# Kernel optimization log

Hardware: AMD Instinct MI355X
Metric: run time of the kernel (lower is better)

The kernel has to match this reference:

```python
import jax, jax.numpy as jnp
import numpy as np

B, N, DIM, H = 4, 2048, 1024, 8
HD = DIM // H
SCALE = HD ** -0.5


def setup_inputs() -> dict:
    key = jax.random.key(0)
    ks = jax.random.split(key, 9)
    inp = {
        "q": jax.random.normal(ks[0], (B, N, DIM), dtype=jnp.float32),
        "k": jax.random.normal(ks[1], (B, N, DIM), dtype=jnp.float32),
        "v": jax.random.normal(ks[2], (B, N, DIM), dtype=jnp.float32),
        "trans_mat": jax.random.normal(ks[3], (B, N, N), dtype=jnp.float32),
        # torch Linear weights: [out_features, in_features]; qkv_bias=False
        "Wq": jax.random.normal(ks[4], (DIM, DIM), dtype=jnp.float32) * (DIM ** -0.5),
        "Wk": jax.random.normal(ks[5], (DIM, DIM), dtype=jnp.float32) * (DIM ** -0.5),
        "Wv": jax.random.normal(ks[6], (DIM, DIM), dtype=jnp.float32) * (DIM ** -0.5),
        "Wp": jax.random.normal(ks[7], (DIM, DIM), dtype=jnp.float32) * (DIM ** -0.5),
        "bp": jax.random.normal(ks[8], (DIM,), dtype=jnp.float32) * 0.01,
    }
    return inp


def reference(q, k, v, trans_mat, Wq, Wk, Wv, Wp, bp):
    Bq, Nq, C = q.shape
    # project and split heads: [B, H, N, HD]
    qh = (q @ Wq.T).reshape(Bq, Nq, H, HD).transpose(0, 2, 1, 3)
    kh = (k @ Wk.T).reshape(Bq, -1, H, HD).transpose(0, 2, 1, 3)
    vh = (v @ Wv.T).reshape(Bq, -1, H, HD).transpose(0, 2, 1, 3)
    # scaled scores gated elementwise by trans_mat (broadcast over heads)
    scores = jnp.einsum("bhqd,bhkd->bhqk", qh, kh) * SCALE
    gated = scores * trans_mat[:, None, :, :]
    # softmax over full row, then zero out positions where gated == 0
    sm = jax.nn.softmax(gated, axis=-1)
    attn = jnp.where(gated != 0, sm, jnp.zeros((), dtype=sm.dtype))
    x = jnp.einsum("bhqk,bhkd->bhqd", attn, vh)
    x = x.transpose(0, 2, 1, 3).reshape(Bq, Nq, C)
    return x @ Wp.T + bp
```

## Files before the change

kernel.cpp:

```cpp
#include <hip/hip_runtime.h>
#include <hip/hip_bf16.h>
#include <stdint.h>

#define B_    4
#define N_    2048
#define DIM_  1024
#define H_    8
#define HD_   128
#define MTOK  (B_ * N_)
#define SCALE_  0.08838834764831845f
#define LOG2E_  1.4426950408889634f
#define QSCALE_ (SCALE_ * LOG2E_)

typedef unsigned short u16;
typedef __attribute__((ext_vector_type(4)))  float f32x4;
typedef __attribute__((ext_vector_type(16))) float f32x16;
typedef __attribute__((ext_vector_type(8)))  short s16x8;
typedef __attribute__((ext_vector_type(8)))  u16  u16x8;
typedef __attribute__((ext_vector_type(4)))  u16  u16x4;
typedef __attribute__((ext_vector_type(4)))  unsigned u32x4;

__device__ __forceinline__ u16 f2bf(float f) {
    uint32_t i = __builtin_bit_cast(uint32_t, f);
    return (u16)((i + 0x7FFFu + ((i >> 16) & 1u)) >> 16);
}
__device__ __forceinline__ unsigned pk_bf16(float a, float b) {
    unsigned r;
    asm("v_cvt_pk_bf16_f32 %0, %1, %2" : "=v"(r) : "v"(a), "v"(b));
    return r;
}
__device__ __forceinline__ void pl32_swap(unsigned &a, unsigned &b) {
    asm volatile("v_permlane32_swap_b32 %0, %1" : "+v"(a), "+v"(b));
}
__device__ __forceinline__ void gl_lds16(const u16* g, u16* l) {
    __builtin_amdgcn_global_load_lds((const __attribute__((address_space(1))) void*)g,
                                     (__attribute__((address_space(3))) void*)l,
                                     16, 0, 0);
}

__global__ __launch_bounds__(256) void cvt_f32_bf16(const float* __restrict__ src,
                                                    u16* __restrict__ dst, int n) {
    int i = (blockIdx.x * 256 + threadIdx.x) * 4;
    int stride = gridDim.x * 256 * 4;
    for (; i < n; i += stride) {
        float4 v = *(const float4*)(src + i);
        u16x4 o;
        o.x = f2bf(v.x); o.y = f2bf(v.y); o.z = f2bf(v.z); o.w = f2bf(v.w);
        *(u16x4*)(dst + i) = o;
    }
}

__global__ __launch_bounds__(256) void cvt3(const float* __restrict__ q,
                                            const float* __restrict__ k,
                                            const float* __restrict__ v,
                                            u16* __restrict__ qb,
                                            u16* __restrict__ kb,
                                            u16* __restrict__ vb) {
    const float* s = blockIdx.y == 0 ? q : blockIdx.y == 1 ? k : v;
    u16* d = blockIdx.y == 0 ? qb : blockIdx.y == 1 ? kb : vb;
    int i = (blockIdx.x * 256 + threadIdx.x) * 8;
    float4 a = *(const float4*)(s + i);
    float4 b = *(const float4*)(s + i + 4);
    u32x4 w = {pk_bf16(a.x, a.y), pk_bf16(a.z, a.w), pk_bf16(b.x, b.y), pk_bf16(b.z, b.w)};
    *(u16x8*)(d + i) = __builtin_bit_cast(u16x8, w);
}

__global__ __launch_bounds__(256) void cvt_w4(const float* __restrict__ s0,
                                              const float* __restrict__ s1,
                                              const float* __restrict__ s2,
                                              const float* __restrict__ s3,
                                              u16* __restrict__ dst) {
    const float* s = blockIdx.y == 0 ? s0 : blockIdx.y == 1 ? s1 : blockIdx.y == 2 ? s2 : s3;
    u16* d = dst + (size_t)blockIdx.y * (DIM_ * DIM_);
    int i = (blockIdx.x * 256 + threadIdx.x) * 8;
    float4 a = *(const float4*)(s + i);
    float4 b = *(const float4*)(s + i + 4);
    u32x4 w = {pk_bf16(a.x, a.y), pk_bf16(a.z, a.w), pk_bf16(b.x, b.y), pk_bf16(b.z, b.w)};
    *(u16x8*)(d + i) = __builtin_bit_cast(u16x8, w);
}

__global__ __launch_bounds__(256) void transpose_f32(const float* __restrict__ in,
                                                     float* __restrict__ out) {
    __shared__ float t[64][65];
    const int r0 = blockIdx.y * 64, c0 = blockIdx.x * 64;
    const float* ib = in + (size_t)blockIdx.z * N_ * N_;
    float* ob = out + (size_t)blockIdx.z * N_ * N_;
    const int lr = threadIdx.x >> 4;
    const int lc = threadIdx.x & 15;
    #pragma unroll
    for (int i = 0; i < 4; i++) {
        int row = i * 16 + lr;
        float4 v = *(const float4*)(ib + (size_t)(r0 + row) * N_ + c0 + lc * 4);
        t[row][lc * 4 + 0] = v.x; t[row][lc * 4 + 1] = v.y;
        t[row][lc * 4 + 2] = v.z; t[row][lc * 4 + 3] = v.w;
    }
    __syncthreads();
    #pragma unroll
    for (int i = 0; i < 4; i++) {
        int row = i * 16 + lr;
        float4 w;
        w.x = t[lc * 4 + 0][row]; w.y = t[lc * 4 + 1][row];
        w.z = t[lc * 4 + 2][row]; w.w = t[lc * 4 + 3][row];
        *(float4*)(ob + (size_t)(c0 + row) * N_ + r0 + lc * 4) = w;
    }
}

template <int MODE>
__global__ __launch_bounds__(256) void gemm_bt(const u16* __restrict__ A,
                                               const u16* __restrict__ Bt,
                                               void* __restrict__ Cout,
                                               const float* __restrict__ bias,
                                               float scale, int M, int NN, int K) {
    __shared__ __align__(16) u16 lga[128 * 64];
    __shared__ __align__(16) u16 lgb[128 * 64];
    const int tid  = threadIdx.x;
    const int lane = tid & 63, wave = tid >> 6;
    const int wm = wave >> 1, wn = wave & 1;
    int lin = blockIdx.x + gridDim.x * blockIdx.y;
    int w   = (lin & 7) * 64 + (lin >> 3);
    const int row0 = (w >> 3) * 128, col0 = (w & 7) * 128;

    f32x4 acc[4][4] = {};

    auto stageLds = [&](const u16* G, u16* L, int rowbase, int k0) {
        #pragma unroll
        for (int i = 0; i < 4; i++) {
            int rb = wave * 32 + i * 8;
            int r  = rb + (lane >> 3);
            int cc = (lane & 7) ^ (lane >> 3);
            gl_lds16(G + (size_t)(rowbase + r) * K + k0 + cc * 8, L + rb * 64);
        }
    };

    for (int k0 = 0; k0 < K; k0 += 64) {
        stageLds(A,  lga, row0, k0);
        stageLds(Bt, lgb, col0, k0);
        __syncthreads();
        #pragma unroll
        for (int kk = 0; kk < 2; kk++) {
            s16x8 af[4], bfr[4];
            #pragma unroll
            for (int mi = 0; mi < 4; mi++) {
                int r = wm * 64 + mi * 16 + (lane & 15);
                int sc = (kk * 4 + (lane >> 4)) ^ (lane & 7);
                af[mi] = *(const s16x8*)(&lga[r * 64 + sc * 8]);
            }
            #pragma unroll
            for (int ni = 0; ni < 4; ni++) {
                int r = wn * 64 + ni * 16 + (lane & 15);
                int sc = (kk * 4 + (lane >> 4)) ^ (lane & 7);
                bfr[ni] = *(const s16x8*)(&lgb[r * 64 + sc * 8]);
            }
            #pragma unroll
            for (int mi = 0; mi < 4; mi++)
                #pragma unroll
                for (int ni = 0; ni < 4; ni++)
                    acc[mi][ni] = __builtin_amdgcn_mfma_f32_16x16x32_bf16(
                        af[mi], bfr[ni], acc[mi][ni], 0, 0, 0);
        }
        __syncthreads();
    }

    #pragma unroll
    for (int mi = 0; mi < 4; mi++) {
        #pragma unroll
        for (int ni = 0; ni < 4; ni++) {
            #pragma unroll
            for (int r = 0; r < 4; r++) {
                int grow = row0 + wm * 64 + mi * 16 + ((lane >> 4) << 2) + r;
                int gcol = col0 + wn * 64 + ni * 16 + (lane & 15);
                float vv = acc[mi][ni][r];
                if (MODE == 2) {
                    ((float*)Cout)[(size_t)grow * NN + gcol] = vv + bias[gcol];
                } else {
                    vv *= scale;
                    int bb = grow >> 11, n = grow & (N_ - 1);
                    int hh = gcol >> 7,  d = gcol & (HD_ - 1);
                    size_t idx = (MODE == 0)
                        ? ((size_t)(bb * H_ + hh) * N_ + n) * HD_ + d
                        : ((size_t)(bb * H_ + hh) * HD_ + d) * N_ + n;
                    ((u16*)Cout)[idx] = f2bf(vv);
                }
            }
        }
    }
}

__global__ __launch_bounds__(256, 2) void attn_swapped(const u16* __restrict__ Qh,
                                                       const u16* __restrict__ Kh,
                                                       const u16* __restrict__ Vt,
                                                       const float* __restrict__ transT,
                                                       u16* __restrict__ xout) {
    __shared__ __align__(16) u16 kt[2][64 * 128];
    __shared__ __align__(16) u16 vt[2][128 * 64];

    const int tid = threadIdx.x, lane = tid & 63, wave = tid >> 6;
    const int lq = lane & 31, hl = lane >> 5;

    int lin = blockIdx.x + 16 * (blockIdx.y + 8 * blockIdx.z);
    int nl  = (lin & 7) * 64 + (lin >> 3);
    const int qt = nl & 15, hh = (nl >> 4) & 7, b = nl >> 7;
    const int q0 = qt * 128 + wave * 32;
    const int q  = q0 + lq;

    const u16* Qbh = Qh + (size_t)(b * H_ + hh) * N_ * HD_;
    const u16* Kbh = Kh + (size_t)(b * H_ + hh) * N_ * HD_;
    const u16* Vbh = Vt + (size_t)(b * H_ + hh) * HD_ * N_;
    const float* tTq = transT + (size_t)b * N_ * N_ + q;

    s16x8 qf[8];
    #pragma unroll
    for (int s = 0; s < 8; s++)
        qf[s] = *(const s16x8*)(Qbh + (size_t)q * HD_ + s * 16 + hl * 8);

    auto stageKV = [&](int kv0, int bi) {
        #pragma unroll
        for (int i = 0; i < 4; i++) {
            int rk = wave * 16 + i * 4 + (lane >> 4);
            int ck = (lane & 15) ^ (rk & 15) ^ ((rk & 16) >> 2);
            gl_lds16(Kbh + (size_t)(kv0 + rk) * HD_ + ck * 8,
                     &kt[bi][(wave * 16 + i * 4) * 128]);
            int rv = wave * 32 + i * 8 + (lane >> 3);
            int cv = (lane & 7) ^ (rv & 7) ^ ((rv >> 3) & 3);
            gl_lds16(Vbh + (size_t)rv * N_ + kv0 + cv * 8,
                     &vt[bi][(wave * 32 + i * 8) * 64]);
        }
    };

    const int mKl = (lq & 15) ^ ((lq & 16) >> 2);
    const int mVl = (lq & 7) ^ ((lq >> 3) & 3);

    float m = -3.0e38f, l = 0.f;
    f32x16 aoT[4] = {};

    stageKV(0, 0);
    __syncthreads();

    for (int it = 0; it < N_ / 64; it++) {
        const int kv0 = it * 64, cur = it & 1;
        if (it + 1 < N_ / 64) stageKV(kv0 + 64, cur ^ 1);

        float tt[2][16];
        #pragma unroll
        for (int ni = 0; ni < 2; ni++)
            #pragma unroll
            for (int idx = 0; idx < 16; idx++) {
                int kv = (idx & 3) + 8 * (idx >> 2) + 4 * hl + 32 * ni;
                tt[ni][idx] = tTq[(size_t)(kv0 + kv) * N_];
            }

        f32x16 sT[2] = {};
        __builtin_amdgcn_s_setprio(1);
        #pragma unroll
        for (int s = 0; s < 8; s++)
            #pragma unroll
            for (int ni = 0; ni < 2; ni++) {
                int r = ni * 32 + lq;
                int slot = (2 * s + hl) ^ mKl;
                s16x8 kf = *(const s16x8*)(&kt[cur][r * 128 + slot * 8]);
                sT[ni] = __builtin_amdgcn_mfma_f32_32x32x16_bf16(kf, qf[s], sT[ni], 0, 0, 0);
            }
        __builtin_amdgcn_s_setprio(0);

        float mx = -3.0e38f;
        #pragma unroll
        for (int ni = 0; ni < 2; ni++)
            #pragma unroll
            for (int idx = 0; idx < 16; idx++) {
                float g = sT[ni][idx] * tt[ni][idx];
                sT[ni][idx] = g;
                mx = fmaxf(mx, g);
            }
        mx = fmaxf(mx, __shfl_xor(mx, 32));

        if (__any(mx > m + 8.0f)) {
            float mn = fmaxf(m, mx);
            float sfv = __builtin_amdgcn_exp2f(m - mn);
            m = mn;
            l *= sfv;
            #pragma unroll
            for (int dt = 0; dt < 4; dt++)
                #pragma unroll
                for (int e = 0; e < 16; e++) aoT[dt][e] *= sfv;
        }

        float rs = 0.f;
        #pragma unroll
        for (int ni = 0; ni < 2; ni++)
            #pragma unroll
            for (int e = 0; e < 16; e++) {
                float g = sT[ni][e];
                float p = __builtin_amdgcn_exp2f(g - m);
                rs += p;
                sT[ni][e] = (g != 0.0f) ? p : 0.0f;
            }
        rs += __shfl_xor(rs, 32);
        l += rs;

        s16x8 pfrag[4];
        #pragma unroll
        for (int sp = 0; sp < 4; sp++) {
            const int ni = sp >> 1;
            const int ru = (2 * sp) & 3, rv2 = (2 * sp + 1) & 3;
            unsigned u0 = pk_bf16(sT[ni][ru * 4 + 0], sT[ni][ru * 4 + 1]);
            unsigned u1 = pk_bf16(sT[ni][ru * 4 + 2], sT[ni][ru * 4 + 3]);
            unsigned v0 = pk_bf16(sT[ni][rv2 * 4 + 0], sT[ni][rv2 * 4 + 1]);
            unsigned v1 = pk_bf16(sT[ni][rv2 * 4 + 2], sT[ni][rv2 * 4 + 3]);
            pl32_swap(u0, v0);
            pl32_swap(u1, v1);
            u32x4 w = {u0, u1, v0, v1};
            pfrag[sp] = __builtin_bit_cast(s16x8, w);
        }

        __builtin_amdgcn_s_setprio(1);
        #pragma unroll
        for (int dt = 0; dt < 4; dt++)
            #pragma unroll
            for (int sp = 0; sp < 4; sp++) {
                int r = dt * 32 + lq;
                int slot = (2 * sp + hl) ^ mVl;
                s16x8 vf = *(const s16x8*)(&vt[cur][r * 64 + slot * 8]);
                aoT[dt] = __builtin_amdgcn_mfma_f32_32x32x16_bf16(vf, pfrag[sp], aoT[dt], 0, 0, 0);
            }
        __builtin_amdgcn_s_setprio(0);
        __syncthreads();
    }

    float inv = 1.0f / l;
    u16* orow = xout + ((size_t)(b * N_ + q)) * DIM_ + hh * HD_;
    #pragma unroll
    for (int dt = 0; dt < 4; dt++)
        #pragma unroll
        for (int r2 = 0; r2 < 4; r2++) {
            u16x4 ov;
            #pragma unroll
            for (int e = 0; e < 4; e++)
                ov[e] = f2bf(aoT[dt][r2 * 4 + e] * inv);
            *(u16x4*)(orow + dt * 32 + r2 * 8 + hl * 4) = ov;
        }
}

__global__ __launch_bounds__(512) void attn_fb(const u16* __restrict__ Qh,
                                               const u16* __restrict__ Kh,
                                               const u16* __restrict__ Vt,
                                               const float* __restrict__ trans,
                                               u16* __restrict__ xout) {
    __shared__ __align__(16) u16 kt[64 * 128];
    __shared__ __align__(16) u16 vt[128 * 64];
    __shared__ __align__(16) u16 plds[8][16 * 72];

    const int tid = threadIdx.x, lane = tid & 63, wave = tid >> 6;
    const int qt = blockIdx.x, h = blockIdx.y, b = blockIdx.z;
    const int qrow_base = qt * 128 + wave * 16;

    const u16* Qbh = Qh + (size_t)(b * H_ + h) * N_ * HD_;
    const u16* Kbh = Kh + (size_t)(b * H_ + h) * N_ * HD_;
    const u16* Vbh = Vt + (size_t)(b * H_ + h) * HD_ * N_;
    const float* trow = trans + (size_t)b * N_ * N_
                      + (size_t)(qrow_base + ((lane >> 4) << 2)) * N_ + (lane & 15);

    s16x8 qf[4];
    {
        int r = qrow_base + (lane & 15);
        #pragma unroll
        for (int kd = 0; kd < 4; kd++)
            qf[kd] = *(const s16x8*)(Qbh + (size_t)r * HD_ + kd * 32 + ((lane >> 4) << 3));
    }
    auto stageKV = [&](int kv0) {
        int rbk = wave * 8, rbv = wave * 16;
        #pragma unroll
        for (int j = 0; j < 2; j++) {
            int c = j * 64 + lane;
            int rk = rbk + (c >> 4), ck = (c & 15) ^ (rk & 15);
            gl_lds16(Kbh + (size_t)(kv0 + rk) * HD_ + ck * 8, kt + rbk * 128 + j * 512);
            int rv = rbv + (c >> 3), cv = (c & 7) ^ (rv & 7);
            gl_lds16(Vbh + (size_t)rv * N_ + kv0 + cv * 8, vt + rbv * 64 + j * 512);
        }
    };

    float m[4], l[4];
    #pragma unroll
    for (int r = 0; r < 4; r++) { m[r] = -3.0e38f; l[r] = 0.f; }
    f32x4 ao[8] = {};

    for (int kv0 = 0; kv0 < N_; kv0 += 64) {
        stageKV(kv0);
        __syncthreads();
        f32x4 s[4] = {};
        #pragma unroll
        for (int kd = 0; kd < 4; kd++)
            #pragma unroll
            for (int ni = 0; ni < 4; ni++) {
                int r = ni * 16 + (lane & 15);
                int sc = (kd * 4 + (lane >> 4)) ^ (lane & 15);
                s16x8 bfr = *(const s16x8*)(&kt[r * 128 + sc * 8]);
                s[ni] = __builtin_amdgcn_mfma_f32_16x16x32_bf16(qf[kd], bfr, s[ni], 0, 0, 0);
            }
        float pmax[4] = {-3.0e38f, -3.0e38f, -3.0e38f, -3.0e38f};
        #pragma unroll
        for (int ni = 0; ni < 4; ni++)
            #pragma unroll
            for (int r = 0; r < 4; r++) {
                float tt = trow[(size_t)r * N_ + kv0 + ni * 16];
                float gg = s[ni][r] * tt;
                s[ni][r] = gg;
                pmax[r] = fmaxf(pmax[r], gg);
            }
        #pragma unroll
        for (int r = 0; r < 4; r++) {
            float p = pmax[r];
            p = fmaxf(p, __shfl_xor(p, 1));
            p = fmaxf(p, __shfl_xor(p, 2));
            p = fmaxf(p, __shfl_xor(p, 4));
            p = fmaxf(p, __shfl_xor(p, 8));
            pmax[r] = p;
        }
        bool need = false;
        #pragma unroll
        for (int r = 0; r < 4; r++) need = need || (pmax[r] > m[r] + 8.0f);
        if (__any(need)) {
            #pragma unroll
            for (int r = 0; r < 4; r++) {
                float mn = fmaxf(m[r], pmax[r]);
                float sfv = __builtin_amdgcn_exp2f(m[r] - mn);
                m[r] = mn; l[r] *= sfv;
                #pragma unroll
                for (int t = 0; t < 8; t++) ao[t][r] *= sfv;
            }
        }
        float rowsum[4] = {0.f, 0.f, 0.f, 0.f};
        u16* pw = &plds[wave][0];
        #pragma unroll
        for (int ni = 0; ni < 4; ni++)
            #pragma unroll
            for (int r = 0; r < 4; r++) {
                float gg = s[ni][r];
                float e = __builtin_amdgcn_exp2f(gg - m[r]);
                rowsum[r] += e;
                float pe = (gg != 0.0f) ? e : 0.0f;
                pw[(((lane >> 4) << 2) + r) * 72 + ni * 16 + (lane & 15)] = f2bf(pe);
            }
        #pragma unroll
        for (int r = 0; r < 4; r++) {
            float ssum = rowsum[r];
            ssum += __shfl_xor(ssum, 1);
            ssum += __shfl_xor(ssum, 2);
            ssum += __shfl_xor(ssum, 4);
            ssum += __shfl_xor(ssum, 8);
            l[r] += ssum;
        }
        #pragma unroll
        for (int kk = 0; kk < 2; kk++) {
            s16x8 pa = *(const s16x8*)(&pw[(lane & 15) * 72 + kk * 32 + ((lane >> 4) << 3)]);
            #pragma unroll
            for (int t = 0; t < 8; t++) {
                int r = t * 16 + (lane & 15);
                int sc = (kk * 4 + (lane >> 4)) ^ (r & 7);
                s16x8 vb = *(const s16x8*)(&vt[r * 64 + sc * 8]);
                ao[t] = __builtin_amdgcn_mfma_f32_16x16x32_bf16(pa, vb, ao[t], 0, 0, 0);
            }
        }
        __syncthreads();
    }
    #pragma unroll
    for (int r = 0; r < 4; r++) {
        float inv = 1.0f / l[r];
        int n = qrow_base + ((lane >> 4) << 2) + r;
        u16* orow = xout + ((size_t)(b * N_ + n)) * DIM_ + h * HD_;
        #pragma unroll
        for (int t = 0; t < 8; t++)
            orow[t * 16 + (lane & 15)] = f2bf(ao[t][r] * inv);
    }
}

extern "C" void kernel_launch(void* const* d_in, const int* in_sizes, int n_in,
                              void* d_out, int out_size, void* d_ws, size_t ws_size,
                              hipStream_t stream) {
    const float* q     = (const float*)d_in[0];
    const float* k     = (const float*)d_in[1];
    const float* v     = (const float*)d_in[2];
    const float* trans = (const float*)d_in[3];
    const float* Wq    = (const float*)d_in[4];
    const float* Wk    = (const float*)d_in[5];
    const float* Wv    = (const float*)d_in[6];
    const float* Wp    = (const float*)d_in[7];
    const float* bp    = (const float*)d_in[8];

    char* ws = (char*)d_ws;
    u16* xb  = (u16*)(ws);
    u16* wqb = (u16*)(ws + (16u << 20));
    u16* wkb = (u16*)(ws + (18u << 20));
    u16* wvb = (u16*)(ws + (20u << 20));
    u16* wpb = (u16*)(ws + (22u << 20));
    u16* QhB = (u16*)(ws + (24u << 20));
    u16* KhB = (u16*)(ws + (40u << 20));
    u16* VtB = (u16*)(ws + (56u << 20));
    u16* qb  = (u16*)(ws + (72u << 20));
    u16* kb  = (u16*)(ws + (88u << 20));
    u16* vb  = (u16*)(ws + (104u << 20));
    float* tT = (float*)(ws + (72u << 20));
    const bool big = ws_size >= (136ull << 20);

    dim3 blk(256);
    cvt_w4<<<dim3(512, 4), blk, 0, stream>>>(Wq, Wk, Wv, Wp, wqb);

    dim3 pg(DIM_ / 128, MTOK / 128);

    if (big) {
        cvt3<<<dim3(4096, 3), blk, 0, stream>>>(q, k, v, qb, kb, vb);
        gemm_bt<0><<<pg, blk, 0, stream>>>(qb, wqb, QhB, nullptr, QSCALE_, MTOK, DIM_, DIM_);
        gemm_bt<0><<<pg, blk, 0, stream>>>(kb, wkb, KhB, nullptr, 1.0f, MTOK, DIM_, DIM_);
        gemm_bt<1><<<pg, blk, 0, stream>>>(vb, wvb, VtB, nullptr, 1.0f, MTOK, DIM_, DIM_);
        transpose_f32<<<dim3(N_ / 64, N_ / 64, B_), blk, 0, stream>>>(trans, tT);
        attn_swapped<<<dim3(16, 8, 4), dim3(256), 0, stream>>>(QhB, KhB, VtB, tT, xb);
    } else {
        u16* tmp = xb;
        cvt_f32_bf16<<<dim3(8192), blk, 0, stream>>>(q, tmp, MTOK * DIM_);
        gemm_bt<0><<<pg, blk, 0, stream>>>(tmp, wqb, QhB, nullptr, QSCALE_, MTOK, DIM_, DIM_);
        cvt_f32_bf16<<<dim3(8192), blk, 0, stream>>>(k, tmp, MTOK * DIM_);
        gemm_bt<0><<<pg, blk, 0, stream>>>(tmp, wkb, KhB, nullptr, 1.0f, MTOK, DIM_, DIM_);
        cvt_f32_bf16<<<dim3(8192), blk, 0, stream>>>(v, tmp, MTOK * DIM_);
        gemm_bt<1><<<pg, blk, 0, stream>>>(tmp, wvb, VtB, nullptr, 1.0f, MTOK, DIM_, DIM_);
        attn_fb<<<dim3(N_ / 128, H_, B_), dim3(512), 0, stream>>>(QhB, KhB, VtB, trans, xb);
    }

    gemm_bt<2><<<pg, blk, 0, stream>>>(xb, wpb, d_out, bp, 1.0f, MTOK, DIM_, DIM_);
}
```

Before: 266.4 us.

## Drop LDS staging in attention and pre-permute gate matrix for vector loads

```diff
diff --git a/kernel.cpp b/kernel.cpp
--- a/kernel.cpp
+++ b/kernel.cpp
@@ -79,29 +79,27 @@
     *(u16x8*)(d + i) = __builtin_bit_cast(u16x8, w);
 }
 
-__global__ __launch_bounds__(256) void transpose_f32(const float* __restrict__ in,
-                                                     float* __restrict__ out) {
-    __shared__ float t[64][65];
-    const int r0 = blockIdx.y * 64, c0 = blockIdx.x * 64;
-    const float* ib = in + (size_t)blockIdx.z * N_ * N_;
-    float* ob = out + (size_t)blockIdx.z * N_ * N_;
-    const int lr = threadIdx.x >> 4;
-    const int lc = threadIdx.x & 15;
+__global__ __launch_bounds__(256) void gate_permute(const float* __restrict__ trans,
+                                                    float* __restrict__ tP) {
+    __shared__ float T[64][68];
+    const int it = blockIdx.x, qc = blockIdx.y, b = blockIdx.z;
+    const float* ib = trans + (size_t)b * N_ * N_;
+    const int q0 = qc * 64;
+    const int lr = threadIdx.x >> 4, lc = threadIdx.x & 15;
     #pragma unroll
     for (int i = 0; i < 4; i++) {
         int row = i * 16 + lr;
-        float4 v = *(const float4*)(ib + (size_t)(r0 + row) * N_ + c0 + lc * 4);
-        t[row][lc * 4 + 0] = v.x; t[row][lc * 4 + 1] = v.y;
-        t[row][lc * 4 + 2] = v.z; t[row][lc * 4 + 3] = v.w;
+        f32x4 v = *(const f32x4*)(ib + (size_t)(q0 + row) * N_ + it * 64 + lc * 4);
+        *(f32x4*)(&T[row][lc * 4]) = v;
     }
     __syncthreads();
-    #pragma unroll
-    for (int i = 0; i < 4; i++) {
-        int row = i * 16 + lr;
-        float4 w;
-        w.x = t[lc * 4 + 0][row]; w.y = t[lc * 4 + 1][row];
-        w.z = t[lc * 4 + 2][row]; w.w = t[lc * 4 + 3][row];
-        *(float4*)(ob + (size_t)(c0 + row) * N_ + r0 + lc * 4) = w;
+    const int q = threadIdx.x >> 2, hl = (threadIdx.x >> 1) & 1, half = threadIdx.x & 1;
+    float* ob = tP + ((((size_t)(b * 32 + it)) * 2048 + q0 + q) * 2 + hl) * 32 + half * 16;
+    #pragma unroll
+    for (int jj = 0; jj < 4; jj++) {
+        int j0 = half * 16 + jj * 4;
+        int ni = j0 >> 4, r2 = (j0 >> 2) & 3;
+        *(f32x4*)(ob + jj * 4) = *(const f32x4*)(&T[q][32 * ni + 8 * r2 + 4 * hl]);
     }
 }
 
@@ -186,15 +184,12 @@
     }
 }
 
-__global__ __launch_bounds__(256, 2) void attn_swapped(const u16* __restrict__ Qh,
-                                                       const u16* __restrict__ Kh,
-                                                       const u16* __restrict__ Vt,
-                                                       const float* __restrict__ transT,
-                                                       u16* __restrict__ xout) {
-    __shared__ __align__(16) u16 kt[2][64 * 128];
-    __shared__ __align__(16) u16 vt[2][128 * 64];
-
-    const int tid = threadIdx.x, lane = tid & 63, wave = tid >> 6;
+__global__ __launch_bounds__(256) void attn_nolds(const u16* __restrict__ Qh,
+                                                  const u16* __restrict__ Kh,
+                                                  const u16* __restrict__ Vt,
+                                                  const float* __restrict__ tP,
+                                                  u16* __restrict__ xout) {
+    const int lane = threadIdx.x & 63, wave = threadIdx.x >> 6;
     const int lq = lane & 31, hl = lane >> 5;
 
     int lin = blockIdx.x + 16 * (blockIdx.y + 8 * blockIdx.z);
@@ -204,60 +199,34 @@
     const int q  = q0 + lq;
 
     const u16* Qbh = Qh + (size_t)(b * H_ + hh) * N_ * HD_;
-    const u16* Kbh = Kh + (size_t)(b * H_ + hh) * N_ * HD_;
-    const u16* Vbh = Vt + (size_t)(b * H_ + hh) * HD_ * N_;
-    const float* tTq = transT + (size_t)b * N_ * N_ + q;
+    const u16* Kl = Kh + (size_t)(b * H_ + hh) * N_ * HD_ + (size_t)lq * HD_ + hl * 8;
+    const u16* Vl = Vt + (size_t)(b * H_ + hh) * HD_ * N_ + (size_t)lq * N_ + hl * 8;
+    const float* tPl = tP + (((size_t)b * 32 * 2048 + q) * 2 + hl) * 32;
 
     s16x8 qf[8];
     #pragma unroll
     for (int s = 0; s < 8; s++)
         qf[s] = *(const s16x8*)(Qbh + (size_t)q * HD_ + s * 16 + hl * 8);
 
-    auto stageKV = [&](int kv0, int bi) {
-        #pragma unroll
-        for (int i = 0; i < 4; i++) {
-            int rk = wave * 16 + i * 4 + (lane >> 4);
-            int ck = (lane & 15) ^ (rk & 15) ^ ((rk & 16) >> 2);
-            gl_lds16(Kbh + (size_t)(kv0 + rk) * HD_ + ck * 8,
-                     &kt[bi][(wave * 16 + i * 4) * 128]);
-            int rv = wave * 32 + i * 8 + (lane >> 3);
-            int cv = (lane & 7) ^ (rv & 7) ^ ((rv >> 3) & 3);
-            gl_lds16(Vbh + (size_t)rv * N_ + kv0 + cv * 8,
-                     &vt[bi][(wave * 32 + i * 8) * 64]);
-        }
-    };
-
-    const int mKl = (lq & 15) ^ ((lq & 16) >> 2);
-    const int mVl = (lq & 7) ^ ((lq >> 3) & 3);
-
     float m = -3.0e38f, l = 0.f;
     f32x16 aoT[4] = {};
 
-    stageKV(0, 0);
-    __syncthreads();
-
     for (int it = 0; it < N_ / 64; it++) {
-        const int kv0 = it * 64, cur = it & 1;
-        if (it + 1 < N_ / 64) stageKV(kv0 + 64, cur ^ 1);
-
-        float tt[2][16];
-        #pragma unroll
-        for (int ni = 0; ni < 2; ni++)
-            #pragma unroll
-            for (int idx = 0; idx < 16; idx++) {
-                int kv = (idx & 3) + 8 * (idx >> 2) + 4 * hl + 32 * ni;
-                tt[ni][idx] = tTq[(size_t)(kv0 + kv) * N_];
-            }
-
+        const int kv0 = it * 64;
+
+        f32x4 ttv[8];
+        #pragma unroll
+        for (int jj = 0; jj < 8; jj++)
+            ttv[jj] = *(const f32x4*)(tPl + (size_t)it * (2048 * 64) + jj * 4);
+
+        const u16* Kt = Kl + (size_t)kv0 * HD_;
         f32x16 sT[2] = {};
         __builtin_amdgcn_s_setprio(1);
         #pragma unroll
         for (int s = 0; s < 8; s++)
             #pragma unroll
             for (int ni = 0; ni < 2; ni++) {
-                int r = ni * 32 + lq;
-                int slot = (2 * s + hl) ^ mKl;
-                s16x8 kf = *(const s16x8*)(&kt[cur][r * 128 + slot * 8]);
+                s16x8 kf = *(const s16x8*)(Kt + ni * (32 * HD_) + s * 16);
                 sT[ni] = __builtin_amdgcn_mfma_f32_32x32x16_bf16(kf, qf[s], sT[ni], 0, 0, 0);
             }
         __builtin_amdgcn_s_setprio(0);
@@ -267,7 +236,7 @@
         for (int ni = 0; ni < 2; ni++)
             #pragma unroll
             for (int idx = 0; idx < 16; idx++) {
-                float g = sT[ni][idx] * tt[ni][idx];
+                float g = sT[ni][idx] * ttv[(ni << 2) | (idx >> 2)][idx & 3];
                 sT[ni][idx] = g;
                 mx = fmaxf(mx, g);
             }
@@ -312,18 +281,16 @@
             pfrag[sp] = __builtin_bit_cast(s16x8, w);
         }
 
+        const u16* Vtile = Vl + kv0;
         __builtin_amdgcn_s_setprio(1);
         #pragma unroll
         for (int dt = 0; dt < 4; dt++)
             #pragma unroll
             for (int sp = 0; sp < 4; sp++) {
-                int r = dt * 32 + lq;
-                int slot = (2 * sp + hl) ^ mVl;
-                s16x8 vf = *(const s16x8*)(&vt[cur][r * 64 + slot * 8]);
+                s16x8 vf = *(const s16x8*)(Vtile + (size_t)dt * (32 * N_) + sp * 16);
                 aoT[dt] = __builtin_amdgcn_mfma_f32_32x32x16_bf16(vf, pfrag[sp], aoT[dt], 0, 0, 0);
             }
         __builtin_amdgcn_s_setprio(0);
-        __syncthreads();
     }
 
     float inv = 1.0f / l;
@@ -498,7 +465,7 @@
     u16* qb  = (u16*)(ws + (72u << 20));
     u16* kb  = (u16*)(ws + (88u << 20));
     u16* vb  = (u16*)(ws + (104u << 20));
-    float* tT = (float*)(ws + (72u << 20));
+    float* tP = (float*)(ws + (72u << 20));
     const bool big = ws_size >= (136ull << 20);
 
     dim3 blk(256);
@@ -511,8 +478,8 @@
         gemm_bt<0><<<pg, blk, 0, stream>>>(qb, wqb, QhB, nullptr, QSCALE_, MTOK, DIM_, DIM_);
         gemm_bt<0><<<pg, blk, 0, stream>>>(kb, wkb, KhB, nullptr, 1.0f, MTOK, DIM_, DIM_);
         gemm_bt<1><<<pg, blk, 0, stream>>>(vb, wvb, VtB, nullptr, 1.0f, MTOK, DIM_, DIM_);
-        transpose_f32<<<dim3(N_ / 64, N_ / 64, B_), blk, 0, stream>>>(trans, tT);
-        attn_swapped<<<dim3(16, 8, 4), dim3(256), 0, stream>>>(QhB, KhB, VtB, tT, xb);
+        gate_permute<<<dim3(32, 32, B_), blk, 0, stream>>>(trans, tP);
+        attn_nolds<<<dim3(16, 8, 4), blk, 0, stream>>>(QhB, KhB, VtB, tP, xb);
     } else {
         u16* tmp = xb;
         cvt_f32_bf16<<<dim3(8192), blk, 0, stream>>>(q, tmp, MTOK * DIM_);
```

Result: slower. 510.2 us (+91.5%).
